# Optimization experiments

Hardware: AMD Instinct MI355X
Metric: run time of the kernel (lower is better)

## Reference

```python
import jax, jax.numpy as jnp
import numpy as np

IN_COUNT = 1024
OUT_COUNT = 1024
NUM_BASIS = 8
INPUT_ABS_MAX = 1.0
X_MIN = 0.0
X_MAX = 1.0
GAMMA_SCALE = 3.0
BATCH = 4096


def setup_inputs() -> dict:
    key = jax.random.key(0)
    k_x, k_c = jax.random.split(key)
    x = jax.random.normal(k_x, (BATCH, IN_COUNT), dtype=jnp.float32)
    coeffs = 0.01 * jax.random.normal(k_c, (OUT_COUNT, IN_COUNT, NUM_BASIS), dtype=jnp.float32)
    # fixed buffers
    centers_1d = jnp.linspace(X_MIN, X_MAX, NUM_BASIS)
    centers = jnp.broadcast_to(centers_1d[None, :], (IN_COUNT, NUM_BASIS)).astype(jnp.float32)
    delta = (X_MAX - X_MIN) / (NUM_BASIS - 1)
    gamma = GAMMA_SCALE / delta
    slopes = jnp.full((IN_COUNT, NUM_BASIS), gamma, dtype=jnp.float32)
    alpha = jnp.full((IN_COUNT,), (X_MAX - X_MIN) / (2.0 * INPUT_ABS_MAX), dtype=jnp.float32)
    beta = jnp.full((IN_COUNT,), 0.5 * (X_MIN + X_MAX), dtype=jnp.float32)
    return {"x": x, "coeffs": coeffs, "centers": centers, "slopes": slopes, "alpha": alpha, "beta": beta}


def reference(x, coeffs, centers, slopes, alpha, beta):
    # u: (B, in) affine transform with fixed alpha/beta
    u = alpha[None, :] * x + beta[None, :]
    # basis: (B, in, basis) = 0.5*(1+tanh(slope*(u - center)))
    basis = 0.5 * (1.0 + jnp.tanh(slopes[None, :, :] * (u[:, :, None] - centers[None, :, :])))
    # y[b,o] = sum_{i,m} coeffs[o,i,m] * basis[b,i,m]  (fused GEMM over in*basis)
    y = jnp.einsum('bim,oim->bo', basis, coeffs)
    return y
```

## Files before the change

kernel.cpp:

```cpp
#include <hip/hip_runtime.h>
#include <hip/hip_bf16.h>
#include <cstdint>
#include <cstddef>

#define BATCH 4096
#define INC   1024
#define OUTC  1024
#define NB    8
#define KDIM  (INC * NB)

#define BM 256
#define BN 128
#define BKB 64
#define SPLITS 4
#define KZ (KDIM / SPLITS)
#define KSTEPS (KZ / BKB)
#define GRID_BLOCKS ((OUTC / BN) * (BATCH / BM) * SPLITS)

#define EXPAND_BLOCKS  ((BATCH * INC) / 256)
#define QUANT_BLOCKS   OUTC
#define PREP_BLOCKS    (EXPAND_BLOCKS + QUANT_BLOCKS)

typedef int   v4i __attribute__((ext_vector_type(4)));
typedef char  v8c __attribute__((ext_vector_type(8)));
typedef short v8s __attribute__((ext_vector_type(8)));

__device__ __forceinline__ unsigned short f2bf(float f) {
  union { float f; unsigned u; } v; v.f = f;
  unsigned r = v.u + 0x7fffu + ((v.u >> 16) & 1u);
  return (unsigned short)(r >> 16);
}
__device__ __forceinline__ float bf2f(unsigned short h) {
  union { unsigned u; float f; } v; v.u = ((unsigned)h) << 16; return v.f;
}

__device__ __forceinline__ void gld16(const char* g, char* l) {
  __builtin_amdgcn_global_load_lds(
      (const __attribute__((address_space(1))) unsigned int*)g,
      (__attribute__((address_space(3))) unsigned int*)l, 16, 0, 0);
}

__global__ __launch_bounds__(256) void prep_kernel(
    const float* __restrict__ x, const float4* __restrict__ coeffs4,
    const float* __restrict__ centers, const float* __restrict__ slopes,
    const float* __restrict__ alpha, const float* __restrict__ beta,
    char* __restrict__ Ai8, int* __restrict__ Ci8i,
    float* __restrict__ maxrow, int* __restrict__ qcsum) {
  const int blk = blockIdx.x;
  const int tid = threadIdx.x;
  if (blk < EXPAND_BLOCKS) {
    const int idx = blk * 256 + tid;
    const int i = idx & (INC - 1);
    const float u = alpha[i] * x[idx] + beta[i];
    const float s0 = slopes[i * NB];
    const float c0 = centers[i * NB];
    const float c1 = centers[i * NB + 1];
    const float L2E2 = 2.8853900817779268f;
    const float a2 = L2E2 * s0;
    float e = __builtin_amdgcn_exp2f(a2 * (c0 - u));
    const float R = __builtin_amdgcn_exp2f(a2 * (c1 - c0));
    v8c q;
#pragma unroll
    for (int m = 0; m < 8; ++m) {
      float basis = __builtin_amdgcn_rcpf(1.0f + e);
      q[m] = (char)(int)rintf(basis * 254.0f - 127.0f);
      e *= R;
    }
    *(v8c*)(Ai8 + (size_t)idx * 8) = q;
  } else {
    const int o = blk - EXPAND_BLOCKS;
    const float4* row = coeffs4 + (size_t)o * (KDIM / 4);
    float4 v[8];
    float m = 0.0f;
#pragma unroll
    for (int j = 0; j < 8; ++j) {
      v[j] = row[tid + 256 * j];
      m = fmaxf(m, fmaxf(fmaxf(fabsf(v[j].x), fabsf(v[j].y)),
                         fmaxf(fabsf(v[j].z), fabsf(v[j].w))));
    }
#pragma unroll
    for (int off = 32; off; off >>= 1) m = fmaxf(m, __shfl_xor(m, off));
    __shared__ float wm[4];
    __shared__ int   wq[4];
    if ((tid & 63) == 0) wm[tid >> 6] = m;
    __syncthreads();
    const float M = fmaxf(fmaxf(fmaxf(wm[0], wm[1]), fmaxf(wm[2], wm[3])), 1e-30f);
    const float s = 127.0f / M;
    int qs = 0;
#pragma unroll
    for (int j = 0; j < 8; ++j) {
      int q0 = (int)rintf(v[j].x * s), q1 = (int)rintf(v[j].y * s);
      int q2 = (int)rintf(v[j].z * s), q3 = (int)rintf(v[j].w * s);
      Ci8i[(size_t)o * (KDIM / 4) + tid + 256 * j] =
          (q0 & 0xFF) | ((q1 & 0xFF) << 8) | ((q2 & 0xFF) << 16) | ((q3 & 0xFF) << 24);
      qs += q0 + q1 + q2 + q3;
    }
#pragma unroll
    for (int off = 32; off; off >>= 1) qs += __shfl_xor(qs, off);
    if ((tid & 63) == 0) wq[tid >> 6] = qs;
    __syncthreads();
    if (tid == 0) { maxrow[o] = M; qcsum[o] = wq[0] + wq[1] + wq[2] + wq[3]; }
  }
}

__global__ __launch_bounds__(512, 4) void gemm_kernel(
    const char* __restrict__ A, const char* __restrict__ C,
    unsigned short* __restrict__ partials) {
  __shared__ __align__(16) char As[2][BM * BKB];
  __shared__ __align__(16) char Bs[2][BN * BKB];

  const int id = (blockIdx.x & 7) * (GRID_BLOCKS / 8) + (blockIdx.x >> 3);
  const int z  = id >> 7;
  const int p  = id & 127;
  const int by = p >> 3;
  const int bx = p & 7;
  const int bm0 = by * BM;
  const int bn0 = bx * BN;
  const int kt0 = z * KZ;

  const int tid  = threadIdx.x;
  const int wave = tid >> 6;
  const int lane = tid & 63;
  const int quad = lane >> 4;
  const int lm   = lane & 15;
  const int wm   = (wave >> 1) * 64;
  const int wn   = (wave & 1) * 64;

  const int r4 = lane >> 2;
  const int gg = (lane & 3) ^ ((lane >> 3) & 3);

  const char* pA0 = A + (size_t)(bm0 + wave * 32 + r4) * KDIM + kt0 + gg * 16;
  const char* pB0 = C + (size_t)(bn0 + wave * 16 + r4) * KDIM + kt0 + gg * 16;
  const int loA = wave * 32 * BKB;
  const int loB = wave * 16 * BKB;

  v4i acc[4][4] = {};
  const int kx = (quad ^ ((lm >> 1) & 3)) * 16;

#define STAGE(SL)                                                            \
  {                                                                          \
    gld16(pA0,                      As[SL] + loA);                           \
    gld16(pA0 + (size_t)16 * KDIM,  As[SL] + loA + 16 * BKB);                \
    gld16(pB0,                      Bs[SL] + loB);                           \
    pA0 += BKB; pB0 += BKB;                                                  \
  }

  STAGE(0);
  STAGE(1);

  for (int t = 0; t < KSTEPS; ++t) {
    const int cur = t & 1;
    if (t < KSTEPS - 1) {
      asm volatile("s_waitcnt vmcnt(3)" ::: "memory");
    } else {
      asm volatile("s_waitcnt vmcnt(0)" ::: "memory");
    }
    __builtin_amdgcn_sched_barrier(0);
    __builtin_amdgcn_s_barrier();

    const char* cA = As[cur];
    const char* cB = Bs[cur];
    v4i a[4], b[4];
#pragma unroll
    for (int f = 0; f < 4; ++f)
      a[f] = *(const v4i*)(cA + (wm + f * 16 + lm) * BKB + kx);
#pragma unroll
    for (int f = 0; f < 4; ++f)
      b[f] = *(const v4i*)(cB + (wn + f * 16 + lm) * BKB + kx);

    __builtin_amdgcn_s_setprio(1);
#pragma unroll
    for (int fm = 0; fm < 4; ++fm)
#pragma unroll
      for (int fn = 0; fn < 4; ++fn)
        acc[fm][fn] = __builtin_amdgcn_mfma_i32_16x16x64_i8(a[fm], b[fn], acc[fm][fn], 0, 0, 0);
    __builtin_amdgcn_s_setprio(0);

    __builtin_amdgcn_s_barrier();
    if (t < KSTEPS - 2) STAGE(cur);
  }
#undef STAGE

  unsigned short* out = partials + (size_t)z * BATCH * OUTC;
#pragma unroll
  for (int fm = 0; fm < 4; ++fm) {
    const int row0 = bm0 + wm + fm * 16 + quad * 4;
#pragma unroll
    for (int fn = 0; fn < 4; ++fn) {
      const int col = bn0 + wn + fn * 16 + lm;
#pragma unroll
      for (int r = 0; r < 4; ++r)
        out[(size_t)(row0 + r) * OUTC + col] = f2bf((float)acc[fm][fn][r]);
    }
  }
}

__global__ __launch_bounds__(256) void reduce_kernel(
    const unsigned short* __restrict__ P, const float* __restrict__ maxrow,
    const int* __restrict__ qcsum, float* __restrict__ out) {
  const size_t nel = (size_t)BATCH * OUTC;
  const size_t base = ((size_t)blockIdx.x * 256 + threadIdx.x) * 8;
  float s[8] = {};
#pragma unroll
  for (int t = 0; t < SPLITS; ++t) {
    v8s v = *(const v8s*)(P + t * nel + base);
#pragma unroll
    for (int j = 0; j < 8; ++j) s[j] += bf2f((unsigned short)v[j]);
  }
  const int o0 = (int)(base & (OUTC - 1));
  const float inv = 1.0f / 32258.0f;
#pragma unroll
  for (int j = 0; j < 8; ++j) {
    const float M = maxrow[o0 + j];
    const int   Q = qcsum[o0 + j];
    s[j] = M * (s[j] + 127.0f * (float)Q) * inv;
  }
  *(float4*)(out + base)     = float4{s[0], s[1], s[2], s[3]};
  *(float4*)(out + base + 4) = float4{s[4], s[5], s[6], s[7]};
}

extern "C" void kernel_launch(void* const* d_in, const int* in_sizes, int n_in,
                              void* d_out, int out_size, void* d_ws, size_t ws_size,
                              hipStream_t stream) {
  const float* x       = (const float*)d_in[0];
  const float* coeffs  = (const float*)d_in[1];
  const float* centers = (const float*)d_in[2];
  const float* slopes  = (const float*)d_in[3];
  const float* alpha   = (const float*)d_in[4];
  const float* beta    = (const float*)d_in[5];
  float* out = (float*)d_out;

  const size_t a_bytes    = (size_t)BATCH * KDIM;
  const size_t c_bytes    = (size_t)OUTC * KDIM;
  const size_t stat_bytes = OUTC * sizeof(float);
  const size_t qcs_bytes  = OUTC * sizeof(int);
  const size_t part_bytes = (size_t)SPLITS * BATCH * OUTC * 2;
  if (ws_size < a_bytes + c_bytes + stat_bytes + qcs_bytes + part_bytes) return;

  char*  Ai8    = (char*)d_ws;
  char*  Ci8    = Ai8 + a_bytes;
  float* maxrow = (float*)(Ci8 + c_bytes);
  int*   qcsum  = (int*)((char*)maxrow + stat_bytes);
  unsigned short* parts = (unsigned short*)((char*)qcsum + qcs_bytes);

  prep_kernel<<<PREP_BLOCKS, 256, 0, stream>>>(
      x, (const float4*)coeffs, centers, slopes, alpha, beta,
      Ai8, (int*)Ci8, maxrow, qcsum);

  gemm_kernel<<<GRID_BLOCKS, 512, 0, stream>>>(Ai8, Ci8, parts);

  reduce_kernel<<<(int)((size_t)BATCH * OUTC / 8 / 256), 256, 0, stream>>>(
      parts, maxrow, qcsum, out);
}
```

Measured before the change: 151.7 us.

## Store split-K partials in fragment-native layout and transpose in reduce via LDS

The GEMM epilogue now packs pairs of bf16 partials into 32-bit words and writes each wave's accumulator fragment contiguously with 16-byte vector stores, replacing the scattered 2-byte stores. The reduce kernel reads this fragment-ordered layout, sums the splits, applies the dequant scale, and transposes through a padded shared-memory tile so the final fp32 output is written with coalesced float4 stores. This targets the cost of uncoalesced narrow stores in the GEMM epilogue. The price is an extra LDS round trip and more complex indexing in the reduce kernel.

```diff
diff --git a/kernel.cpp b/kernel.cpp
--- a/kernel.cpp
+++ b/kernel.cpp
@@ -21,9 +21,9 @@
 #define QUANT_BLOCKS   OUTC
 #define PREP_BLOCKS    (EXPAND_BLOCKS + QUANT_BLOCKS)
 
-typedef int   v4i __attribute__((ext_vector_type(4)));
-typedef char  v8c __attribute__((ext_vector_type(8)));
-typedef short v8s __attribute__((ext_vector_type(8)));
+typedef int      v4i __attribute__((ext_vector_type(4)));
+typedef unsigned v4u __attribute__((ext_vector_type(4)));
+typedef char     v8c __attribute__((ext_vector_type(8)));
 
 __device__ __forceinline__ unsigned short f2bf(float f) {
   union { float f; unsigned u; } v; v.f = f;
@@ -105,7 +105,7 @@
 
 __global__ __launch_bounds__(512, 4) void gemm_kernel(
     const char* __restrict__ A, const char* __restrict__ C,
-    unsigned short* __restrict__ partials) {
+    unsigned* __restrict__ partials) {
   __shared__ __align__(16) char As[2][BM * BKB];
   __shared__ __align__(16) char Bs[2][BN * BKB];
 
@@ -181,42 +181,78 @@
   }
 #undef STAGE
 
-  unsigned short* out = partials + (size_t)z * BATCH * OUTC;
-#pragma unroll
-  for (int fm = 0; fm < 4; ++fm) {
-    const int row0 = bm0 + wm + fm * 16 + quad * 4;
-#pragma unroll
-    for (int fn = 0; fn < 4; ++fn) {
-      const int col = bn0 + wn + fn * 16 + lm;
-#pragma unroll
-      for (int r = 0; r < 4; ++r)
-        out[(size_t)(row0 + r) * OUTC + col] = f2bf((float)acc[fm][fn][r]);
-    }
-  }
+  unsigned w32[32];
+#pragma unroll
+  for (int fm = 0; fm < 4; ++fm)
+#pragma unroll
+    for (int fn = 0; fn < 4; ++fn)
+#pragma unroll
+      for (int rr = 0; rr < 2; ++rr)
+        w32[fm * 8 + fn * 2 + rr] =
+            (unsigned)f2bf((float)acc[fm][fn][2 * rr]) |
+            ((unsigned)f2bf((float)acc[fm][fn][2 * rr + 1]) << 16);
+
+  unsigned* outp = partials + (((size_t)z * 128 + p) * 8 + wave) * 2048 + lane * 4;
+#pragma unroll
+  for (int c = 0; c < 8; ++c)
+    *(v4u*)(outp + c * 256) = v4u{w32[4 * c], w32[4 * c + 1], w32[4 * c + 2], w32[4 * c + 3]};
 }
 
 __global__ __launch_bounds__(256) void reduce_kernel(
-    const unsigned short* __restrict__ P, const float* __restrict__ maxrow,
+    const unsigned* __restrict__ P, const float* __restrict__ maxrow,
     const int* __restrict__ qcsum, float* __restrict__ out) {
-  const size_t nel = (size_t)BATCH * OUTC;
-  const size_t base = ((size_t)blockIdx.x * 256 + threadIdx.x) * 8;
-  float s[8] = {};
-#pragma unroll
-  for (int t = 0; t < SPLITS; ++t) {
-    v8s v = *(const v8s*)(P + t * nel + base);
-#pragma unroll
-    for (int j = 0; j < 8; ++j) s[j] += bf2f((unsigned short)v[j]);
-  }
-  const int o0 = (int)(base & (OUTC - 1));
+  const int blk = blockIdx.x;
+  const int p = blk >> 3, w = blk & 7;
+  const int bm0 = (p >> 3) * BM, bn0 = (p & 7) * BN;
+  const int B0 = bm0 + (w >> 1) * 64;
+  const int O0 = bn0 + (w & 1) * 64;
+  const int t = threadIdx.x;
+
+  __shared__ float tile[64][65];
+  __shared__ float sM[64];
+  __shared__ float sQ[64];
+  if (t < 64) { sM[t] = maxrow[O0 + t]; sQ[t] = 127.0f * (float)qcsum[O0 + t]; }
+  __syncthreads();
+
+  const size_t base = ((size_t)p * 8 + w) * 2048 + (size_t)t * 8;
+  const size_t zs   = (size_t)128 * 8 * 2048;
+  float slo[8] = {}, shi[8] = {};
+#pragma unroll
+  for (int z = 0; z < SPLITS; ++z) {
+    v4u ua = *(const v4u*)(P + z * zs + base);
+    v4u ub = *(const v4u*)(P + z * zs + base + 4);
+#pragma unroll
+    for (int k = 0; k < 4; ++k) {
+      slo[k]     += bf2f((unsigned short)(ua[k] & 0xFFFFu));
+      shi[k]     += bf2f((unsigned short)(ua[k] >> 16));
+      slo[k + 4] += bf2f((unsigned short)(ub[k] & 0xFFFFu));
+      shi[k + 4] += bf2f((unsigned short)(ub[k] >> 16));
+    }
+  }
   const float inv = 1.0f / 32258.0f;
 #pragma unroll
-  for (int j = 0; j < 8; ++j) {
-    const float M = maxrow[o0 + j];
-    const int   Q = qcsum[o0 + j];
-    s[j] = M * (s[j] + 127.0f * (float)Q) * inv;
-  }
-  *(float4*)(out + base)     = float4{s[0], s[1], s[2], s[3]};
-  *(float4*)(out + base + 4) = float4{s[4], s[5], s[6], s[7]};
+  for (int k = 0; k < 8; ++k) {
+    const int W  = t * 8 + k;
+    const int c  = W >> 8;
+    const int l  = (W >> 2) & 63;
+    const int j  = (c << 2) | (W & 3);
+    const int fm = j >> 3, fn = (j >> 1) & 3, rr = j & 1;
+    const int bl = fm * 16 + (l >> 4) * 4 + rr * 2;
+    const int ol = fn * 16 + (l & 15);
+    const float M = sM[ol], corr = sQ[ol];
+    tile[bl][ol]     = M * (slo[k] + corr) * inv;
+    tile[bl + 1][ol] = M * (shi[k] + corr) * inv;
+  }
+  __syncthreads();
+
+  const int row = t >> 2;
+  const int c0  = (t & 3) * 16;
+  float* op = out + (size_t)(B0 + row) * OUTC + O0 + c0;
+#pragma unroll
+  for (int i = 0; i < 4; ++i) {
+    *(float4*)(op + 4 * i) = float4{tile[row][c0 + 4 * i],     tile[row][c0 + 4 * i + 1],
+                                    tile[row][c0 + 4 * i + 2], tile[row][c0 + 4 * i + 3]};
+  }
 }
 
 extern "C" void kernel_launch(void* const* d_in, const int* in_sizes, int n_in,
@@ -241,7 +277,7 @@
   char*  Ci8    = Ai8 + a_bytes;
   float* maxrow = (float*)(Ci8 + c_bytes);
   int*   qcsum  = (int*)((char*)maxrow + stat_bytes);
-  unsigned short* parts = (unsigned short*)((char*)qcsum + qcs_bytes);
+  unsigned* parts = (unsigned*)((char*)qcsum + qcs_bytes);
 
   prep_kernel<<<PREP_BLOCKS, 256, 0, stream>>>(
       x, (const float4*)coeffs, centers, slopes, alpha, beta,
@@ -249,6 +285,5 @@
 
   gemm_kernel<<<GRID_BLOCKS, 512, 0, stream>>>(Ai8, Ci8, parts);
 
-  reduce_kernel<<<(int)((size_t)BATCH * OUTC / 8 / 256), 256, 0, stream>>>(
-      parts, maxrow, qcsum, out);
-}
+  reduce_kernel<<<128 * 8, 256, 0, stream>>>(parts, maxrow, qcsum, out);
+}
```

Result: slower. 155.6 us (+2.6%).
